# Optimization experiments

Measured on AMD Instinct MI355X. Metric: run time of the kernel, lower is better.

The kernel has to match this reference:

```python
import jax, jax.numpy as jnp
import numpy as np

B, S, D, H = 2, 2048, 1024, 16
DK = D // H


def setup_inputs() -> dict:
    key = jax.random.key(0)
    ks = jax.random.split(key, 11)
    scale = 1.0 / np.sqrt(D)
    inp = {
        "q": jax.random.normal(ks[0], (B, S, D), jnp.float32),
        "k": jax.random.normal(ks[1], (B, S, D), jnp.float32),
        "v": jax.random.normal(ks[2], (B, S, D), jnp.float32),
        "mask": jnp.tril(jnp.ones((S, S), jnp.int32))[None, None],  # causal [1,1,S,S]
        "wq": jax.random.normal(ks[3], (D, D), jnp.float32) * scale,
        "bq": jnp.zeros((D,), jnp.float32),
        "wk": jax.random.normal(ks[4], (D, D), jnp.float32) * scale,
        "bk": jnp.zeros((D,), jnp.float32),
        "wv": jax.random.normal(ks[5], (D, D), jnp.float32) * scale,
        "bv": jnp.zeros((D,), jnp.float32),
        "wo": jax.random.normal(ks[6], (D, D), jnp.float32) * scale,
        "bo": jnp.zeros((D,), jnp.float32),
    }
    return inp


def _split_heads(x):  # [B,S,D] -> [B,H,S,DK]
    return x.reshape(B, S, H, DK).transpose(0, 2, 1, 3)


def reference(q, k, v, mask, wq, bq, wk, bk, wv, bv, wo, bo):
    # projections (nn.Linear: x @ W.T + b)
    query = _split_heads(q @ wq.T + bq)
    key_ = _split_heads(k @ wk.T + bk)
    value = _split_heads(v @ wv.T + bv)
    # scaled dot-product attention, full [B,H,S,S] scores as in source
    scores = jnp.einsum('bhqd,bhkd->bhqk', query, key_) / np.sqrt(DK)
    scores = jnp.where(mask == 0, jnp.float32(-1e9), scores)
    attn = jax.nn.softmax(scores, axis=-1)
    out = jnp.einsum('bhqk,bhkd->bhqd', attn, value)
    out = out.transpose(0, 2, 1, 3).reshape(B, S, D)
    x = out @ wo.T + bo
    return x, attn
```

## Files before the change

### kernel.cpp

```cpp
#include <hip/hip_runtime.h>
#include <hip/hip_bf16.h>

typedef __attribute__((ext_vector_type(8))) __bf16 bf16x8;
typedef __attribute__((ext_vector_type(4))) __bf16 bf16x4;
typedef __attribute__((ext_vector_type(4))) float f32x4;

#define MFMA16(a, b, c) __builtin_amdgcn_mfma_f32_16x16x32_bf16((a), (b), (c), 0, 0, 0)

#define SEQ 2048
#define DIM 1024

__global__ __launch_bounds__(256) void qkv_gemm(
    const float* __restrict__ qI, const float* __restrict__ kI, const float* __restrict__ vI,
    const float* __restrict__ wqI, const float* __restrict__ wkI, const float* __restrict__ wvI,
    const float* __restrict__ bqI, const float* __restrict__ bkI, const float* __restrict__ bvI,
    __bf16* __restrict__ Qp, __bf16* __restrict__ Kp, __bf16* __restrict__ Vt) {
  const int N = 1024, K = 1024;
  int z = blockIdx.z;
  const float* A = (z == 0) ? qI : (z == 1) ? kI : vI;
  const float* W = (z == 0) ? wqI : (z == 1) ? wkI : wvI;
  const float* bias = (z == 0) ? bqI : (z == 1) ? bkI : bvI;

  __shared__ __bf16 As[128][40];
  __shared__ __bf16 Bs[128][40];

  int tid = threadIdx.x;
  int wave = tid >> 6, lane = tid & 63;
  int quad = lane >> 4, l16 = lane & 15;
  int wm = (wave >> 1) * 64, wn = (wave & 1) * 64;
  int m0 = blockIdx.y * 128, n0 = blockIdx.x * 128;
  int sr = tid >> 3;
  int sc = (tid & 7) * 4;

  f32x4 acc[4][4] = {};

  float4 pa[4], pw[4];
#pragma unroll
  for (int i = 0; i < 4; i++) {
    int r = sr + i * 32;
    pa[i] = *(const float4*)&A[(size_t)(m0 + r) * K + sc];
    pw[i] = *(const float4*)&W[(size_t)(n0 + r) * K + sc];
  }

  for (int k0 = 0; k0 < K; k0 += 32) {
    __syncthreads();
#pragma unroll
    for (int i = 0; i < 4; i++) {
      int r = sr + i * 32;
      bf16x4 ah = {(__bf16)pa[i].x, (__bf16)pa[i].y, (__bf16)pa[i].z, (__bf16)pa[i].w};
      bf16x4 wh = {(__bf16)pw[i].x, (__bf16)pw[i].y, (__bf16)pw[i].z, (__bf16)pw[i].w};
      *(bf16x4*)&As[r][sc] = ah;
      *(bf16x4*)&Bs[r][sc] = wh;
    }
    __syncthreads();
    if (k0 + 32 < K) {
#pragma unroll
      for (int i = 0; i < 4; i++) {
        int r = sr + i * 32;
        pa[i] = *(const float4*)&A[(size_t)(m0 + r) * K + k0 + 32 + sc];
        pw[i] = *(const float4*)&W[(size_t)(n0 + r) * K + k0 + 32 + sc];
      }
    }
    bf16x8 af[4], bfv[4];
#pragma unroll
    for (int i = 0; i < 4; i++) af[i] = *(bf16x8*)&As[wm + i * 16 + l16][quad * 8];
#pragma unroll
    for (int j = 0; j < 4; j++) bfv[j] = *(bf16x8*)&Bs[wn + j * 16 + l16][quad * 8];
#pragma unroll
    for (int i = 0; i < 4; i++)
#pragma unroll
      for (int j = 0; j < 4; j++) acc[i][j] = MFMA16(af[i], bfv[j], acc[i][j]);
  }

#pragma unroll
  for (int j = 0; j < 4; j++) {
    int col = n0 + wn + j * 16 + l16;
    float bj = bias[col];
    if (z == 2) {
#pragma unroll
      for (int i = 0; i < 4; i++) {
        int row0 = m0 + wm + i * 16 + quad * 4;
        int bb = row0 >> 11, s = row0 & 2047;
        bf16x4 pv = {(__bf16)(acc[i][j][0] + bj), (__bf16)(acc[i][j][1] + bj),
                     (__bf16)(acc[i][j][2] + bj), (__bf16)(acc[i][j][3] + bj)};
        *(bf16x4*)&Vt[((size_t)bb * 1024 + col) * SEQ + s] = pv;
      }
    } else {
      __bf16* C = (z == 0) ? Qp : Kp;
      float scale = (z == 0) ? 0.125f : 1.0f;
#pragma unroll
      for (int i = 0; i < 4; i++)
#pragma unroll
        for (int r = 0; r < 4; r++) {
          int row = m0 + wm + i * 16 + quad * 4 + r;
          C[(size_t)row * N + col] = (__bf16)((acc[i][j][r] + bj) * scale);
        }
    }
  }
}

__global__ __launch_bounds__(256) void out_gemm(
    const __bf16* __restrict__ A, const float* __restrict__ W,
    const float* __restrict__ bias, float* __restrict__ C) {
  const int N = 1024, K = 1024;
  __shared__ __bf16 As[128][40];
  __shared__ __bf16 Bs[128][40];

  int tid = threadIdx.x;
  int wave = tid >> 6, lane = tid & 63;
  int quad = lane >> 4, l16 = lane & 15;
  int wm = (wave >> 1) * 64, wn = (wave & 1) * 64;
  int m0 = blockIdx.y * 128, n0 = blockIdx.x * 128;
  int sr = tid >> 3;
  int sc = (tid & 7) * 4;

  f32x4 acc[4][4] = {};

  bf16x4 pa[4];
  float4 pw[4];
#pragma unroll
  for (int i = 0; i < 4; i++) {
    int r = sr + i * 32;
    pa[i] = *(const bf16x4*)&A[(size_t)(m0 + r) * K + sc];
    pw[i] = *(const float4*)&W[(size_t)(n0 + r) * K + sc];
  }

  for (int k0 = 0; k0 < K; k0 += 32) {
    __syncthreads();
#pragma unroll
    for (int i = 0; i < 4; i++) {
      int r = sr + i * 32;
      bf16x4 wh = {(__bf16)pw[i].x, (__bf16)pw[i].y, (__bf16)pw[i].z, (__bf16)pw[i].w};
      *(bf16x4*)&As[r][sc] = pa[i];
      *(bf16x4*)&Bs[r][sc] = wh;
    }
    __syncthreads();
    if (k0 + 32 < K) {
#pragma unroll
      for (int i = 0; i < 4; i++) {
        int r = sr + i * 32;
        pa[i] = *(const bf16x4*)&A[(size_t)(m0 + r) * K + k0 + 32 + sc];
        pw[i] = *(const float4*)&W[(size_t)(n0 + r) * K + k0 + 32 + sc];
      }
    }
    bf16x8 af[4], bfv[4];
#pragma unroll
    for (int i = 0; i < 4; i++) af[i] = *(bf16x8*)&As[wm + i * 16 + l16][quad * 8];
#pragma unroll
    for (int j = 0; j < 4; j++) bfv[j] = *(bf16x8*)&Bs[wn + j * 16 + l16][quad * 8];
#pragma unroll
    for (int i = 0; i < 4; i++)
#pragma unroll
      for (int j = 0; j < 4; j++) acc[i][j] = MFMA16(af[i], bfv[j], acc[i][j]);
  }

#pragma unroll
  for (int j = 0; j < 4; j++) {
    int col = n0 + wn + j * 16 + l16;
    float bj = bias[col];
#pragma unroll
    for (int i = 0; i < 4; i++)
#pragma unroll
      for (int r = 0; r < 4; r++) {
        int row = m0 + wm + i * 16 + quad * 4 + r;
        C[(size_t)row * N + col] = acc[i][j][r] + bj;
      }
  }
}

__global__ __launch_bounds__(256) void attn_fused(
    const __bf16* __restrict__ Qp, const __bf16* __restrict__ Kp,
    const __bf16* __restrict__ Vt, float* __restrict__ attn,
    __bf16* __restrict__ Oc) {
  int bh = blockIdx.y;
  int b = bh >> 4;
  int hofs = (bh & 15) * 64;
  int q0 = blockIdx.x * 64;

  int tid = threadIdx.x;
  int wave = tid >> 6, lane = tid & 63;
  int quad = lane >> 4, l16 = lane & 15;

  __shared__ __bf16 Qs[64][72];
  __shared__ __bf16 Ks[128][72];
  __shared__ __bf16 Vts[64][136];
  __shared__ __bf16 Ps[64][136];

  const size_t rowbase = (size_t)b * SEQ;
  const size_t vtbase = (size_t)bh * 64 * SEQ;

#pragma unroll
  for (int it = 0; it < 2; it++) {
    int flat = tid * 8 + it * 2048;
    int r = flat >> 6, c = flat & 63;
    *(bf16x8*)&Qs[r][c] = *(const bf16x8*)&Qp[(rowbase + q0 + r) * DIM + hofs + c];
  }
  __syncthreads();

  int qg = q0 + wave * 16 + l16;
  bf16x8 qfrag0 = *(bf16x8*)&Qs[wave * 16 + l16][quad * 8];
  bf16x8 qfrag1 = *(bf16x8*)&Qs[wave * 16 + l16][32 + quad * 8];

  float m_i = -1e30f, l_i = 0.f;
  int ktmax = (q0 + 63) >> 7;

  for (int kt = 0; kt <= ktmax; kt++) {
    int k0 = kt << 7;
    __syncthreads();
#pragma unroll
    for (int it = 0; it < 4; it++) {
      int flat = tid * 8 + it * 2048;
      int r = flat >> 6, c = flat & 63;
      *(bf16x8*)&Ks[r][c] = *(const bf16x8*)&Kp[(rowbase + k0 + r) * DIM + hofs + c];
    }
    __syncthreads();

    f32x4 sacc[8] = {};
#pragma unroll
    for (int t = 0; t < 8; t++) {
      bf16x8 a0 = *(bf16x8*)&Ks[t * 16 + l16][quad * 8];
      bf16x8 a1 = *(bf16x8*)&Ks[t * 16 + l16][32 + quad * 8];
      sacc[t] = MFMA16(a0, qfrag0, sacc[t]);
      sacc[t] = MFMA16(a1, qfrag1, sacc[t]);
    }

    bool diag = (kt == ktmax);
    float sv[32];
    float mx = -1e30f;
#pragma unroll
    for (int t = 0; t < 8; t++)
#pragma unroll
      for (int r = 0; r < 4; r++) {
        float s = sacc[t][r];
        int k = k0 + t * 16 + quad * 4 + r;
        if (diag && k > qg) s = -1e30f;
        sv[t * 4 + r] = s;
        mx = fmaxf(mx, s);
      }
    mx = fmaxf(mx, __shfl_xor(mx, 16));
    mx = fmaxf(mx, __shfl_xor(mx, 32));
    float mn = fmaxf(m_i, mx);
    float sum = 0.f;
#pragma unroll
    for (int i = 0; i < 32; i++) sum += __expf(sv[i] - mn);
    sum += __shfl_xor(sum, 16);
    sum += __shfl_xor(sum, 32);
    l_i = l_i * __expf(m_i - mn) + sum;
    m_i = mn;
  }

  float rl = 1.f / l_i;
  f32x4 oacc[4] = {};
  float* attn_bh = attn + (size_t)bh * SEQ * SEQ;
  float* attn_row = attn_bh + (size_t)qg * SEQ;

  for (int kt = 0; kt < SEQ / 128; kt++) {
    int k0 = kt << 7;
    if (kt <= ktmax) {
      __syncthreads();
#pragma unroll
      for (int it = 0; it < 4; it++) {
        int flat = tid * 8 + it * 2048;
        int r = flat >> 6, c = flat & 63;
        *(bf16x8*)&Ks[r][c] = *(const bf16x8*)&Kp[(rowbase + k0 + r) * DIM + hofs + c];
        int d = flat >> 7, c2 = flat & 127;
        *(bf16x8*)&Vts[d][c2] = *(const bf16x8*)&Vt[vtbase + (size_t)d * SEQ + k0 + c2];
      }
      __syncthreads();

      f32x4 sacc[8] = {};
#pragma unroll
      for (int t = 0; t < 8; t++) {
        bf16x8 a0 = *(bf16x8*)&Ks[t * 16 + l16][quad * 8];
        bf16x8 a1 = *(bf16x8*)&Ks[t * 16 + l16][32 + quad * 8];
        sacc[t] = MFMA16(a0, qfrag0, sacc[t]);
        sacc[t] = MFMA16(a1, qfrag1, sacc[t]);
      }

      bool diag = (kt == ktmax);
#pragma unroll
      for (int t = 0; t < 8; t++) {
        float p[4];
#pragma unroll
        for (int r = 0; r < 4; r++) {
          int k = k0 + t * 16 + quad * 4 + r;
          float s = sacc[t][r];
          p[r] = (!diag || k <= qg) ? __expf(s - m_i) * rl : 0.f;
        }
        *(float4*)&attn_row[k0 + t * 16 + quad * 4] = make_float4(p[0], p[1], p[2], p[3]);
        bf16x4 ph = {(__bf16)p[0], (__bf16)p[1], (__bf16)p[2], (__bf16)p[3]};
        *(bf16x4*)&Ps[wave * 16 + l16][t * 16 + quad * 4] = ph;
      }
      __syncthreads();

#pragma unroll
      for (int ks = 0; ks < 4; ks++) {
        bf16x8 a = *(bf16x8*)&Ps[wave * 16 + l16][ks * 32 + quad * 8];
#pragma unroll
        for (int dt = 0; dt < 4; dt++) {
          bf16x8 bb = *(bf16x8*)&Vts[dt * 16 + l16][ks * 32 + quad * 8];
          oacc[dt] = MFMA16(a, bb, oacc[dt]);
        }
      }
    } else {
      float4 z4 = make_float4(0.f, 0.f, 0.f, 0.f);
#pragma unroll
      for (int i = 0; i < 8; i++) {
        int f4 = tid + i * 256;
        int r = f4 >> 5;
        int c = (f4 & 31) * 4;
        *(float4*)&attn_bh[(size_t)(q0 + r) * SEQ + k0 + c] = z4;
      }
    }
  }

#pragma unroll
  for (int dt = 0; dt < 4; dt++)
#pragma unroll
    for (int rr = 0; rr < 4; rr++) {
      int row = q0 + wave * 16 + quad * 4 + rr;
      Oc[(rowbase + row) * DIM + hofs + dt * 16 + l16] = (__bf16)oacc[dt][rr];
    }
}

extern "C" void kernel_launch(void* const* d_in, const int* in_sizes, int n_in,
                              void* d_out, int out_size, void* d_ws, size_t ws_size,
                              hipStream_t stream) {
  const float* q = (const float*)d_in[0];
  const float* k = (const float*)d_in[1];
  const float* v = (const float*)d_in[2];
  const float* wq = (const float*)d_in[4];
  const float* bq = (const float*)d_in[5];
  const float* wk = (const float*)d_in[6];
  const float* bk = (const float*)d_in[7];
  const float* wv = (const float*)d_in[8];
  const float* bv = (const float*)d_in[9];
  const float* wo = (const float*)d_in[10];
  const float* bo = (const float*)d_in[11];

  float* xout = (float*)d_out;
  float* attn = xout + (size_t)2 * SEQ * DIM;

  __bf16* Qp = (__bf16*)d_ws;
  __bf16* Kp = Qp + (size_t)2 * SEQ * DIM;
  __bf16* Vt = Kp + (size_t)2 * SEQ * DIM;
  __bf16* Oc = Vt + (size_t)2 * SEQ * DIM;

  dim3 blk(256);
  dim3 g1(8, 32, 3);
  qkv_gemm<<<g1, blk, 0, stream>>>(q, k, v, wq, wk, wv, bq, bk, bv, Qp, Kp, Vt);

  dim3 g2(32, 32);
  attn_fused<<<g2, blk, 0, stream>>>(Qp, Kp, Vt, attn, Oc);

  dim3 g3(8, 32);
  out_gemm<<<g3, blk, 0, stream>>>(Oc, wo, bo, xout);
}
```

Baseline: 794.0 us.

## Load K/V/Q MFMA fragments directly from global memory, drop LDS staging and barriers

Removes the shared-memory staging of Q, K and V tiles in the attention kernel and has each wave load its MFMA operand fragments straight from global memory, relying on L1/L2 caching. Block-wide barriers are replaced by a per-wave LDS wait, since each wave only reads back its own rows of Ps. This is meant to cut barrier stalls and LDS traffic and raise occupancy, at the cost of redundant global loads across the four waves and less coalesced accesses.

```diff
diff --git a/kernel.cpp b/kernel.cpp
--- a/kernel.cpp
+++ b/kernel.cpp
@@ -181,45 +181,31 @@
   int wave = tid >> 6, lane = tid & 63;
   int quad = lane >> 4, l16 = lane & 15;
 
-  __shared__ __bf16 Qs[64][72];
-  __shared__ __bf16 Ks[128][72];
-  __shared__ __bf16 Vts[64][136];
   __shared__ __bf16 Ps[64][136];
 
   const size_t rowbase = (size_t)b * SEQ;
   const size_t vtbase = (size_t)bh * 64 * SEQ;
 
-#pragma unroll
-  for (int it = 0; it < 2; it++) {
-    int flat = tid * 8 + it * 2048;
-    int r = flat >> 6, c = flat & 63;
-    *(bf16x8*)&Qs[r][c] = *(const bf16x8*)&Qp[(rowbase + q0 + r) * DIM + hofs + c];
-  }
-  __syncthreads();
-
   int qg = q0 + wave * 16 + l16;
-  bf16x8 qfrag0 = *(bf16x8*)&Qs[wave * 16 + l16][quad * 8];
-  bf16x8 qfrag1 = *(bf16x8*)&Qs[wave * 16 + l16][32 + quad * 8];
+
+  const __bf16* qp = Qp + (rowbase + qg) * DIM + hofs + quad * 8;
+  bf16x8 qfrag0 = *(const bf16x8*)qp;
+  bf16x8 qfrag1 = *(const bf16x8*)(qp + 32);
+
+  const __bf16* kb = Kp + (rowbase + l16) * DIM + hofs + quad * 8;
+  const __bf16* vb = Vt + vtbase + (size_t)l16 * SEQ + quad * 8;
 
   float m_i = -1e30f, l_i = 0.f;
   int ktmax = (q0 + 63) >> 7;
 
   for (int kt = 0; kt <= ktmax; kt++) {
     int k0 = kt << 7;
-    __syncthreads();
-#pragma unroll
-    for (int it = 0; it < 4; it++) {
-      int flat = tid * 8 + it * 2048;
-      int r = flat >> 6, c = flat & 63;
-      *(bf16x8*)&Ks[r][c] = *(const bf16x8*)&Kp[(rowbase + k0 + r) * DIM + hofs + c];
-    }
-    __syncthreads();
-
     f32x4 sacc[8] = {};
 #pragma unroll
     for (int t = 0; t < 8; t++) {
-      bf16x8 a0 = *(bf16x8*)&Ks[t * 16 + l16][quad * 8];
-      bf16x8 a1 = *(bf16x8*)&Ks[t * 16 + l16][32 + quad * 8];
+      const __bf16* kp = kb + (size_t)(k0 + t * 16) * DIM;
+      bf16x8 a0 = *(const bf16x8*)kp;
+      bf16x8 a1 = *(const bf16x8*)(kp + 32);
       sacc[t] = MFMA16(a0, qfrag0, sacc[t]);
       sacc[t] = MFMA16(a1, qfrag1, sacc[t]);
     }
@@ -257,22 +243,12 @@
   for (int kt = 0; kt < SEQ / 128; kt++) {
     int k0 = kt << 7;
     if (kt <= ktmax) {
-      __syncthreads();
-#pragma unroll
-      for (int it = 0; it < 4; it++) {
-        int flat = tid * 8 + it * 2048;
-        int r = flat >> 6, c = flat & 63;
-        *(bf16x8*)&Ks[r][c] = *(const bf16x8*)&Kp[(rowbase + k0 + r) * DIM + hofs + c];
-        int d = flat >> 7, c2 = flat & 127;
-        *(bf16x8*)&Vts[d][c2] = *(const bf16x8*)&Vt[vtbase + (size_t)d * SEQ + k0 + c2];
-      }
-      __syncthreads();
-
       f32x4 sacc[8] = {};
 #pragma unroll
       for (int t = 0; t < 8; t++) {
-        bf16x8 a0 = *(bf16x8*)&Ks[t * 16 + l16][quad * 8];
-        bf16x8 a1 = *(bf16x8*)&Ks[t * 16 + l16][32 + quad * 8];
+        const __bf16* kp = kb + (size_t)(k0 + t * 16) * DIM;
+        bf16x8 a0 = *(const bf16x8*)kp;
+        bf16x8 a1 = *(const bf16x8*)(kp + 32);
         sacc[t] = MFMA16(a0, qfrag0, sacc[t]);
         sacc[t] = MFMA16(a1, qfrag1, sacc[t]);
       }
@@ -291,14 +267,14 @@
         bf16x4 ph = {(__bf16)p[0], (__bf16)p[1], (__bf16)p[2], (__bf16)p[3]};
         *(bf16x4*)&Ps[wave * 16 + l16][t * 16 + quad * 4] = ph;
       }
-      __syncthreads();
+      asm volatile("s_waitcnt lgkmcnt(0)" ::: "memory");
 
 #pragma unroll
       for (int ks = 0; ks < 4; ks++) {
         bf16x8 a = *(bf16x8*)&Ps[wave * 16 + l16][ks * 32 + quad * 8];
 #pragma unroll
         for (int dt = 0; dt < 4; dt++) {
-          bf16x8 bb = *(bf16x8*)&Vts[dt * 16 + l16][ks * 32 + quad * 8];
+          bf16x8 bb = *(const bf16x8*)(vb + (size_t)(dt * 16) * SEQ + k0 + ks * 32);
           oacc[dt] = MFMA16(a, bb, oacc[dt]);
         }
       }
```

After: 993.2 us. +25.1%, slower.
